# Kernel tuning notes

Hardware: AMD Instinct MI355X
Metric: run time of the kernel (lower is better)

## Reference

```python
import jax, jax.numpy as jnp
import numpy as np

D_MODEL = 1024
NUM_HEADS = 16
HEAD_DIM = D_MODEL // NUM_HEADS


def setup_inputs() -> dict:
    key = jax.random.key(0)
    ks = jax.random.split(key, 9)
    B, S, D = 4, 2048, D_MODEL
    scale = 1.0 / np.sqrt(D)
    x = jax.random.normal(ks[0], (B, S, D), dtype=jnp.float32)
    wq = jax.random.normal(ks[1], (D, D), dtype=jnp.float32) * scale
    wk = jax.random.normal(ks[2], (D, D), dtype=jnp.float32) * scale
    wv = jax.random.normal(ks[3], (D, D), dtype=jnp.float32) * scale
    wo = jax.random.normal(ks[4], (D, D), dtype=jnp.float32) * scale
    bq = jax.random.normal(ks[5], (D,), dtype=jnp.float32) * 0.02
    bk = jax.random.normal(ks[6], (D,), dtype=jnp.float32) * 0.02
    bv = jax.random.normal(ks[7], (D,), dtype=jnp.float32) * 0.02
    bo = jax.random.normal(ks[8], (D,), dtype=jnp.float32) * 0.02
    return {"x": x, "wq": wq, "bq": bq, "wk": wk, "bk": bk,
            "wv": wv, "bv": bv, "wo": wo, "bo": bo}


def _split_heads(t):  # [B,S,D] -> [B,H,S,Dh]
    B, S, _ = t.shape
    return t.reshape(B, S, NUM_HEADS, HEAD_DIM).transpose(0, 2, 1, 3)


def reference(x, wq, bq, wk, bk, wv, bv, wo, bo):
    B, S, D = x.shape
    q = _split_heads(x @ wq + bq)  # [B,H,S,Dh]
    k = _split_heads(x @ wk + bk)
    v = _split_heads(x @ wv + bv)
    scores = jnp.einsum("bhqd,bhkd->bhqk", q, k) / jnp.sqrt(
        jnp.asarray(HEAD_DIM, dtype=x.dtype))
    causal = jnp.tril(jnp.ones((S, S), dtype=bool))  # [S,S]
    scores = jnp.where(causal, scores, jnp.finfo(scores.dtype).min)
    attn = jax.nn.softmax(scores, axis=-1)
    ctx = jnp.einsum("bhqk,bhkd->bhqd", attn, v)  # [B,H,S,Dh]
    ctx = ctx.transpose(0, 2, 1, 3).reshape(B, S, D)
    return ctx @ wo + bo
```

## Files before the change

### kernel.cpp

```cpp
#include <hip/hip_runtime.h>
#include <hip/hip_bf16.h>
#include <stdint.h>

#define DMODEL 1024
#define NH 16
#define DH 64
#define BATCH 4
#define SEQ 2048

#if __has_builtin(__builtin_amdgcn_exp2f)
#define EXP2F(x) __builtin_amdgcn_exp2f(x)
#else
#define EXP2F(x) exp2f(x)
#endif

typedef __attribute__((ext_vector_type(8))) short short8;
typedef __attribute__((ext_vector_type(4))) float f32x4;
typedef __attribute__((ext_vector_type(4))) ushort ushort4v;

__device__ __forceinline__ ushort f2bf(float f) {
    union { float f; unsigned u; } v; v.f = f;
    unsigned r = v.u + 0x7fffu + ((v.u >> 16) & 1u);
    return (ushort)(r >> 16);
}

__global__ __launch_bounds__(256) void prep_inputs(
    const float* __restrict__ x, ushort* __restrict__ xbf,
    const float* __restrict__ s0, const float* __restrict__ s1,
    const float* __restrict__ s2, const float* __restrict__ s3,
    ushort* __restrict__ d0, ushort* __restrict__ d1,
    ushort* __restrict__ d2, ushort* __restrict__ d3) {
    __shared__ ushort tile[64][65];
    const int bid = blockIdx.x;
    if (bid < 4096) {
        const size_t i = ((size_t)bid * 256 + threadIdx.x) * 8;
        float4 a = *(const float4*)(x + i);
        float4 b = *(const float4*)(x + i + 4);
        short8 r;
        r[0] = (short)f2bf(a.x); r[1] = (short)f2bf(a.y);
        r[2] = (short)f2bf(a.z); r[3] = (short)f2bf(a.w);
        r[4] = (short)f2bf(b.x); r[5] = (short)f2bf(b.y);
        r[6] = (short)f2bf(b.z); r[7] = (short)f2bf(b.w);
        *(short8*)(xbf + i) = r;
        return;
    }
    const int r = bid - 4096;
    const int z = r >> 8;
    const float* src = (z == 0) ? s0 : (z == 1) ? s1 : (z == 2) ? s2 : s3;
    ushort* dst = (z == 0) ? d0 : (z == 1) ? d1 : (z == 2) ? d2 : d3;
    const int bx = (r & 15) * 64;
    const int by = ((r >> 4) & 15) * 64;
    const int tx = threadIdx.x & 63, ty = threadIdx.x >> 6;
    #pragma unroll
    for (int i = 0; i < 64; i += 4)
        tile[ty + i][tx] = f2bf(src[(size_t)(by + ty + i) * DMODEL + bx + tx]);
    __syncthreads();
    #pragma unroll
    for (int i = 0; i < 64; i += 4)
        dst[(size_t)(bx + ty + i) * DMODEL + by + tx] = tile[tx][ty + i];
}

#define BK 64
#define NT 16

template <int MODE>
__global__ __launch_bounds__(256, 2) void gemm_tile(
    const ushort* __restrict__ A, const ushort* __restrict__ Bt,
    const float* __restrict__ b0, const float* __restrict__ b1,
    const float* __restrict__ b2,
    void* __restrict__ o0v, void* __restrict__ o1v, void* __restrict__ o2v) {
    __shared__ __align__(16) ushort lds[32768];
    const int tid  = threadIdx.x;
    const int lane = tid & 63;
    const int wv   = tid >> 6;

    const int bid = blockIdx.x;
    const int by  = ((bid & 7) << 3) | ((bid >> 3) & 7);
    const int bx  = bid >> 6;
    const int mBase = by * 128, nBase = bx * 128;

    const int wm = (wv >> 1) * 64;
    const int wn = (wv & 1) * 64;
    const int frow = lane & 15;
    const int fq   = lane >> 4;
    const int r7x  = frow & 7;
    const int swk0 = (fq ^ r7x) << 3;
    const int swk1 = ((4 + fq) ^ r7x) << 3;

    const int trow = tid >> 3;
    const int tcho = ((tid & 7) ^ (trow & 7)) * 8;
    const ushort* gA = A  + (size_t)(mBase + trow) * DMODEL + tcho;
    const ushort* gB = Bt + (size_t)(nBase + trow) * DMODEL + tcho;
    const int ldsw = wv * 512;

    f32x4 acc[4][4];
    #pragma unroll
    for (int i = 0; i < 4; ++i)
        #pragma unroll
        for (int j = 0; j < 4; ++j) acc[i][j] = (f32x4){0.f, 0.f, 0.f, 0.f};

#define STG(gp, off) __builtin_amdgcn_global_load_lds( \
    (const __attribute__((address_space(1))) void*)(gp), \
    (__attribute__((address_space(3))) void*)&lds[(off) + ldsw], 16, 0, 0)
#define STAGE_A(sb, u, g) STG(gA + (size_t)(g) * 32 * DMODEL + (u) * BK, \
                              (sb) + (g) * 2048)
#define STAGE_B(sb, u, g) STG(gB + (size_t)(g) * 32 * DMODEL + (u) * BK, \
                              (sb) + 8192 + (g) * 2048)
#define STAGE_ALL(sb, u) { \
    STAGE_A(sb, u, 0); STAGE_A(sb, u, 1); STAGE_A(sb, u, 2); STAGE_A(sb, u, 3); \
    STAGE_B(sb, u, 0); STAGE_B(sb, u, 1); STAGE_B(sb, u, 2); STAGE_B(sb, u, 3); }

    STAGE_ALL(0, 0);
    asm volatile("s_waitcnt vmcnt(0)" ::: "memory");
    __builtin_amdgcn_s_barrier();

    #pragma unroll 1
    for (int u = 0; u < NT; ++u) {
        const int cb = (u & 1) * 16384;
        const int nb = 16384 - cb;

        if (u + 1 < NT) STAGE_ALL(nb, u + 1);

        const ushort* bufA = &lds[cb + wm * 64];
        const ushort* bufB = &lds[cb + 8192 + wn * 64];
        short8 af[4][2], bf[4][2];
        #pragma unroll
        for (int f = 0; f < 4; ++f) {
            const int ro = (f * 16 + frow) * 64;
            af[f][0] = *(const short8*)&bufA[ro + swk0];
            af[f][1] = *(const short8*)&bufA[ro + swk1];
        }
        #pragma unroll
        for (int j = 0; j < 4; ++j) {
            const int ro = (j * 16 + frow) * 64;
            bf[j][0] = *(const short8*)&bufB[ro + swk0];
            bf[j][1] = *(const short8*)&bufB[ro + swk1];
        }
        __builtin_amdgcn_s_setprio(1);
        #pragma unroll
        for (int f = 0; f < 4; ++f)
            #pragma unroll
            for (int j = 0; j < 4; ++j)
                #pragma unroll
                for (int ks = 0; ks < 2; ++ks)
                    acc[f][j] = __builtin_amdgcn_mfma_f32_16x16x32_bf16(
                        af[f][ks], bf[j][ks], acc[f][j], 0, 0, 0);
        __builtin_amdgcn_s_setprio(0);

        asm volatile("s_waitcnt vmcnt(0)" ::: "memory");
        __builtin_amdgcn_s_barrier();
    }
#undef STG
#undef STAGE_A
#undef STAGE_B
#undef STAGE_ALL

    const int orow = fq * 4;
    const int ocol = frow;

    if (MODE == 1) {
        #pragma unroll
        for (int i = 0; i < 4; ++i)
            #pragma unroll
            for (int j = 0; j < 4; ++j)
                #pragma unroll
                for (int r = 0; r < 4; ++r) {
                    const int m = mBase + wm + i * 16 + orow + r;
                    const int n = nBase + wn + j * 16 + ocol;
                    ((float*)o0v)[(size_t)m * DMODEL + n] = acc[i][j][r] + b0[n];
                }
        return;
    }

    __syncthreads();
    ushort* o0 = (ushort*)o0v; ushort* o1 = (ushort*)o1v; ushort* o2 = (ushort*)o2v;
    ushort* sw = &lds[wv * 1152];
    const int mat = nBase >> 10;
    const int nb0 = (nBase & 1023) + wn;
    const int hb  = nb0 >> 6;
    const float* bp = (mat == 0) ? b0 : ((mat == 1) ? b1 : b2);
    float bj[4];
    #pragma unroll
    for (int j = 0; j < 4; ++j) bj[j] = bp[nb0 + j * 16 + ocol];
    const int mrow = mBase + wm;
    const int bbq = mrow >> 11;
    const int s0w = mrow & 2047;
    const float qscale = (mat == 0) ? 0.1803368801f : 1.0f;

    if (mat < 2) {
        ushort* obase = ((mat == 0) ? o0 : o1) +
                        ((size_t)(bbq * NH + hb) * SEQ + s0w) * DH;
        const int row = lane >> 2, cc = lane & 3;
        #pragma unroll
        for (int i = 0; i < 4; ++i) {
            #pragma unroll
            for (int j = 0; j < 4; ++j)
                #pragma unroll
                for (int r = 0; r < 4; ++r)
                    sw[(orow + r) * 72 + j * 16 + ocol] =
                        f2bf((acc[i][j][r] + bj[j]) * qscale);
            asm volatile("s_waitcnt lgkmcnt(0)" ::: "memory");
            #pragma unroll
            for (int p = 0; p < 2; ++p) {
                short8 v8 = *(const short8*)&sw[row * 72 + cc * 8 + p * 32];
                *(short8*)&obase[(size_t)(i * 16 + row) * DH + cc * 8 + p * 32] = v8;
            }
            asm volatile("s_waitcnt lgkmcnt(0)" ::: "memory");
        }
    } else {
        const int rowd = lane >> 2, scl = lane & 3;
        #pragma unroll
        for (int j = 0; j < 4; ++j) {
            #pragma unroll
            for (int ii = 0; ii < 4; ++ii)
                #pragma unroll
                for (int r = 0; r < 4; ++r)
                    sw[ocol * 72 + ii * 16 + orow + r] = f2bf(acc[ii][j][r] + bj[j]);
            asm volatile("s_waitcnt lgkmcnt(0)" ::: "memory");
            ushort* vbase = o2 + ((size_t)(bbq * NH + hb) * DH + j * 16 + rowd) * SEQ + s0w;
            #pragma unroll
            for (int p = 0; p < 2; ++p) {
                short8 v8 = *(const short8*)&sw[rowd * 72 + scl * 8 + p * 32];
                *(short8*)&vbase[scl * 8 + p * 32] = v8;
            }
            asm volatile("s_waitcnt lgkmcnt(0)" ::: "memory");
        }
    }
}

#define PSTR 72
__global__ __launch_bounds__(512, 2) void flash_attn(
    const ushort* __restrict__ Q, const ushort* __restrict__ K,
    const ushort* __restrict__ Vt, ushort* __restrict__ ctx) {
    __shared__ __align__(16) ushort Ks[3][4096];
    __shared__ __align__(16) ushort Vs[3][4096];
    __shared__ __align__(16) ushort plds[8][16 * PSTR];
    const int tid  = threadIdx.x;
    const int lane = tid & 63;
    const int wv   = tid >> 6;
    const int bh   = blockIdx.x & 63;
    const int Jp   = blockIdx.x >> 6;
    const int bb = bh >> 4, h = bh & 15;

    const ushort* Qb = Q + (size_t)bh * SEQ * DH;
    const ushort* Kb = K + (size_t)bh * SEQ * DH;
    const ushort* Vb = Vt + (size_t)bh * DH * SEQ;

    const int frow = lane & 15;
    const int fq   = lane >> 4;
    const int trow = tid >> 3;
    const int tcho = ((tid & 7) ^ (trow & 7)) * 8;
    const int ldsw = wv * 512;

    short8 ones;
    #pragma unroll
    for (int i = 0; i < 8; ++i) ones[i] = (short)0x3F80;

#define FA_STG(gp, lp) __builtin_amdgcn_global_load_lds( \
    (const __attribute__((address_space(1))) void*)(gp), \
    (__attribute__((address_space(3))) void*)(lp), 16, 0, 0)
#define FA_STAGE(kt, buf) { \
    FA_STG(Kb + (size_t)((kt) * 64 + trow) * DH + tcho, &Ks[buf][ldsw]); \
    FA_STG(Vb + (size_t)trow * SEQ + (kt) * 64 + tcho, &Vs[buf][ldsw]); }

    #pragma unroll 1
    for (int half = 0; half < 2; ++half) {
        const int J = half ? (15 - Jp) : Jp;
        const int ktmax = 2 * J + 1;
        const int q0 = J * 128 + (wv >> 2) * 64 + (wv & 3) * 16;
        const int qmax = q0 + 15;

        short8 qf[2];
        #pragma unroll
        for (int ks = 0; ks < 2; ++ks)
            qf[ks] = *(const short8*)&Qb[(size_t)(q0 + frow) * DH + ks * 32 + fq * 8];

        f32x4 o[4], lacc;
        #pragma unroll
        for (int t = 0; t < 4; ++t) o[t] = (f32x4){0.f, 0.f, 0.f, 0.f};
        lacc = (f32x4){0.f, 0.f, 0.f, 0.f};

        FA_STAGE(0, 0);
        FA_STAGE(1, 1);
        asm volatile("s_waitcnt vmcnt(2)" ::: "memory");
        __builtin_amdgcn_s_barrier();

        #pragma unroll 1
        for (int kt = 0; kt <= ktmax; ++kt) {
            const int k0 = kt * 64;
            const int cur = kt % 3;
            const bool more = (kt + 2 <= ktmax);
            if (more) FA_STAGE(kt + 2, (kt + 2) % 3);
            const ushort* Ksc = Ks[cur];
            const ushort* Vsc = Vs[cur];

            if (k0 <= qmax) {
            if (k0 + 64 <= q0) {
                f32x4 sacc[4];
                #pragma unroll
                for (int nt = 0; nt < 4; ++nt) sacc[nt] = (f32x4){0.f, 0.f, 0.f, 0.f};
                #pragma unroll
                for (int nt = 0; nt < 4; ++nt) {
                    const int row = nt * 16 + frow, r7 = row & 7;
                    #pragma unroll
                    for (int ks = 0; ks < 2; ++ks) {
                        short8 kf = *(const short8*)
                            &Ksc[(row >> 3) * 512 + r7 * 64 + (((ks * 4 + fq) ^ r7) * 8)];
                        sacc[nt] = __builtin_amdgcn_mfma_f32_16x16x32_bf16(kf, qf[ks],
                                                                          sacc[nt], 0, 0, 0);
                    }
                }
                #pragma unroll
                for (int nt = 0; nt < 4; ++nt) {
                    float p0 = EXP2F(sacc[nt][0]);
                    float p1 = EXP2F(sacc[nt][1]);
                    float p2 = EXP2F(sacc[nt][2]);
                    float p3 = EXP2F(sacc[nt][3]);
                    uint2 dw;
                    dw.x = __builtin_amdgcn_perm(__float_as_uint(p1), __float_as_uint(p0),
                                                 0x07060302u);
                    dw.y = __builtin_amdgcn_perm(__float_as_uint(p3), __float_as_uint(p2),
                                                 0x07060302u);
                    *(uint2*)&plds[wv][frow * PSTR + nt * 16 + fq * 4] = dw;
                }
                asm volatile("s_waitcnt lgkmcnt(0)" ::: "memory");
                #pragma unroll
                for (int kc = 0; kc < 2; ++kc) {
                    short8 pf = *(const short8*)&plds[wv][frow * PSTR + kc * 32 + fq * 8];
                    lacc = __builtin_amdgcn_mfma_f32_16x16x32_bf16(ones, pf, lacc, 0, 0, 0);
                    __builtin_amdgcn_s_setprio(1);
                    #pragma unroll
                    for (int t = 0; t < 4; ++t) {
                        const int row = t * 16 + frow, r7 = row & 7;
                        short8 vf = *(const short8*)
                            &Vsc[(row >> 3) * 512 + r7 * 64 + (((kc * 4 + fq) ^ r7) * 8)];
                        o[t] = __builtin_amdgcn_mfma_f32_16x16x32_bf16(vf, pf, o[t], 0, 0, 0);
                    }
                    __builtin_amdgcn_s_setprio(0);
                }
            } else {
                const int qrow = q0 + frow;
                f32x4 sacc[4];
                #pragma unroll
                for (int nt = 0; nt < 4; ++nt) sacc[nt] = (f32x4){0.f, 0.f, 0.f, 0.f};
                #pragma unroll
                for (int nt = 0; nt < 4; ++nt)
                    if (k0 + nt * 16 <= qmax) {
                        const int row = nt * 16 + frow, r7 = row & 7;
                        #pragma unroll
                        for (int ks = 0; ks < 2; ++ks) {
                            short8 kf = *(const short8*)
                                &Ksc[(row >> 3) * 512 + r7 * 64 + (((ks * 4 + fq) ^ r7) * 8)];
                            sacc[nt] = __builtin_amdgcn_mfma_f32_16x16x32_bf16(kf, qf[ks],
                                                                              sacc[nt], 0, 0, 0);
                        }
                    }
                #pragma unroll
                for (int nt = 0; nt < 4; ++nt) {
                    uint2 dw; dw.x = 0u; dw.y = 0u;
                    if (k0 + nt * 16 <= qmax) {
                        float pp[4];
                        #pragma unroll
                        for (int r = 0; r < 4; ++r) {
                            const float e = EXP2F(sacc[nt][r]);
                            pp[r] = (k0 + nt * 16 + fq * 4 + r <= qrow) ? e : 0.f;
                        }
                        dw.x = __builtin_amdgcn_perm(__float_as_uint(pp[1]),
                                                     __float_as_uint(pp[0]), 0x07060302u);
                        dw.y = __builtin_amdgcn_perm(__float_as_uint(pp[3]),
                                                     __float_as_uint(pp[2]), 0x07060302u);
                    }
                    *(uint2*)&plds[wv][frow * PSTR + nt * 16 + fq * 4] = dw;
                }
                asm volatile("s_waitcnt lgkmcnt(0)" ::: "memory");
                #pragma unroll
                for (int kc = 0; kc < 2; ++kc) {
                    if (k0 + kc * 32 <= qmax) {
                        short8 pf = *(const short8*)&plds[wv][frow * PSTR + kc * 32 + fq * 8];
                        lacc = __builtin_amdgcn_mfma_f32_16x16x32_bf16(ones, pf, lacc, 0, 0, 0);
                        #pragma unroll
                        for (int t = 0; t < 4; ++t) {
                            const int row = t * 16 + frow, r7 = row & 7;
                            short8 vf = *(const short8*)
                                &Vsc[(row >> 3) * 512 + r7 * 64 + (((kc * 4 + fq) ^ r7) * 8)];
                            o[t] = __builtin_amdgcn_mfma_f32_16x16x32_bf16(vf, pf, o[t], 0, 0, 0);
                        }
                    }
                }
            }
            }

            if (more) { asm volatile("s_waitcnt lgkmcnt(0) vmcnt(2)" ::: "memory"); }
            else      { asm volatile("s_waitcnt lgkmcnt(0) vmcnt(0)" ::: "memory"); }
            __builtin_amdgcn_s_barrier();
        }

        const float inv = 1.0f / lacc[0];
        const int qrow = q0 + frow;
        ushort* cp = ctx + (size_t)(bb * SEQ + qrow) * DMODEL + h * DH;
        #pragma unroll
        for (int t = 0; t < 4; ++t) {
            ushort4v ov;
            #pragma unroll
            for (int r = 0; r < 4; ++r) ov[r] = f2bf(o[t][r] * inv);
            *(ushort4v*)&cp[t * 16 + fq * 4] = ov;
        }
    }
#undef FA_STG
#undef FA_STAGE
}

extern "C" void kernel_launch(void* const* d_in, const int* in_sizes, int n_in,
                              void* d_out, int out_size, void* d_ws, size_t ws_size,
                              hipStream_t stream) {
    const float* x  = (const float*)d_in[0];
    const float* wq = (const float*)d_in[1];
    const float* bq = (const float*)d_in[2];
    const float* wk = (const float*)d_in[3];
    const float* bk = (const float*)d_in[4];
    const float* wvp = (const float*)d_in[5];
    const float* bv = (const float*)d_in[6];
    const float* wo = (const float*)d_in[7];
    const float* bo = (const float*)d_in[8];
    float* out = (float*)d_out;
    ushort* ws = (ushort*)d_ws;

    const size_t QSZ = (size_t)BATCH * NH * SEQ * DH;
    ushort* xbf   = ws;
    ushort* qws   = ws + QSZ;
    ushort* kws   = ws + 2 * QSZ;
    ushort* vtws  = ws + 3 * QSZ;
    ushort* ctxws = ws + 4 * QSZ;
    ushort* wtqkv = ws + 5 * QSZ;
    ushort* wto   = wtqkv + 3 * (size_t)DMODEL * DMODEL;

    dim3 tb(256);
    prep_inputs<<<dim3(5120), tb, 0, stream>>>(
        x, xbf, wq, wk, wvp, wo,
        wtqkv, wtqkv + (size_t)DMODEL * DMODEL, wtqkv + 2 * (size_t)DMODEL * DMODEL, wto);

    gemm_tile<0><<<dim3(1536), tb, 0, stream>>>(xbf, wtqkv, bq, bk, bv,
                                                qws, kws, vtws);
    flash_attn<<<dim3(512), dim3(512), 0, stream>>>(qws, kws, vtws, ctxws);
    gemm_tile<1><<<dim3(512), tb, 0, stream>>>(ctxws, wto, bo, nullptr, nullptr,
                                               out, nullptr, nullptr);
}
```

Measured before the change: 220.0 us.

## Give each flash-attention wave two query tiles to reuse K/V fragments

The attention block shrinks from 8 to 4 waves. Each wave now handles 32 query rows as two 16-row tiles, so every K and V fragment read from LDS feeds two MFMAs instead of one. Each thread issues twice as many global-to-LDS staging loads per tile, and the vmcnt waits are adjusted to match. The aim is to halve LDS fragment traffic per MFMA. The cost is higher register pressure and fewer waves per block to hide latency.

```diff
diff --git a/kernel.cpp b/kernel.cpp
--- a/kernel.cpp
+++ b/kernel.cpp
@@ -229,12 +229,12 @@
 }
 
 #define PSTR 72
-__global__ __launch_bounds__(512, 2) void flash_attn(
+__global__ __launch_bounds__(256, 2) void flash_attn(
     const ushort* __restrict__ Q, const ushort* __restrict__ K,
     const ushort* __restrict__ Vt, ushort* __restrict__ ctx) {
     __shared__ __align__(16) ushort Ks[3][4096];
     __shared__ __align__(16) ushort Vs[3][4096];
-    __shared__ __align__(16) ushort plds[8][16 * PSTR];
+    __shared__ __align__(16) ushort plds[4][2][16 * PSTR];
     const int tid  = threadIdx.x;
     const int lane = tid & 63;
     const int wv   = tid >> 6;
@@ -261,28 +261,36 @@
     (__attribute__((address_space(3))) void*)(lp), 16, 0, 0)
 #define FA_STAGE(kt, buf) { \
     FA_STG(Kb + (size_t)((kt) * 64 + trow) * DH + tcho, &Ks[buf][ldsw]); \
-    FA_STG(Vb + (size_t)trow * SEQ + (kt) * 64 + tcho, &Vs[buf][ldsw]); }
+    FA_STG(Kb + (size_t)((kt) * 64 + 32 + trow) * DH + tcho, &Ks[buf][2048 + ldsw]); \
+    FA_STG(Vb + (size_t)trow * SEQ + (kt) * 64 + tcho, &Vs[buf][ldsw]); \
+    FA_STG(Vb + (size_t)(32 + trow) * SEQ + (kt) * 64 + tcho, &Vs[buf][2048 + ldsw]); }
 
     #pragma unroll 1
     for (int half = 0; half < 2; ++half) {
         const int J = half ? (15 - Jp) : Jp;
         const int ktmax = 2 * J + 1;
-        const int q0 = J * 128 + (wv >> 2) * 64 + (wv & 3) * 16;
-        const int qmax = q0 + 15;
-
-        short8 qf[2];
-        #pragma unroll
-        for (int ks = 0; ks < 2; ++ks)
-            qf[ks] = *(const short8*)&Qb[(size_t)(q0 + frow) * DH + ks * 32 + fq * 8];
-
-        f32x4 o[4], lacc;
-        #pragma unroll
-        for (int t = 0; t < 4; ++t) o[t] = (f32x4){0.f, 0.f, 0.f, 0.f};
-        lacc = (f32x4){0.f, 0.f, 0.f, 0.f};
+        const int q0 = J * 128 + wv * 32;
+        const int qmax0 = q0 + 15, qmax1 = q0 + 31;
+
+        short8 qf[2][2];
+        #pragma unroll
+        for (int qt = 0; qt < 2; ++qt)
+            #pragma unroll
+            for (int ks = 0; ks < 2; ++ks)
+                qf[qt][ks] = *(const short8*)
+                    &Qb[(size_t)(q0 + qt * 16 + frow) * DH + ks * 32 + fq * 8];
+
+        f32x4 o[2][4], lacc[2];
+        #pragma unroll
+        for (int qt = 0; qt < 2; ++qt) {
+            #pragma unroll
+            for (int t = 0; t < 4; ++t) o[qt][t] = (f32x4){0.f, 0.f, 0.f, 0.f};
+            lacc[qt] = (f32x4){0.f, 0.f, 0.f, 0.f};
+        }
 
         FA_STAGE(0, 0);
         FA_STAGE(1, 1);
-        asm volatile("s_waitcnt vmcnt(2)" ::: "memory");
+        asm volatile("s_waitcnt vmcnt(4)" ::: "memory");
         __builtin_amdgcn_s_barrier();
 
         #pragma unroll 1
@@ -294,11 +302,14 @@
             const ushort* Ksc = Ks[cur];
             const ushort* Vsc = Vs[cur];
 
-            if (k0 <= qmax) {
+            if (k0 <= qmax1) {
             if (k0 + 64 <= q0) {
-                f32x4 sacc[4];
-                #pragma unroll
-                for (int nt = 0; nt < 4; ++nt) sacc[nt] = (f32x4){0.f, 0.f, 0.f, 0.f};
+                f32x4 sacc[2][4];
+                #pragma unroll
+                for (int qt = 0; qt < 2; ++qt)
+                    #pragma unroll
+                    for (int nt = 0; nt < 4; ++nt)
+                        sacc[qt][nt] = (f32x4){0.f, 0.f, 0.f, 0.f};
                 #pragma unroll
                 for (int nt = 0; nt < 4; ++nt) {
                     const int row = nt * 16 + frow, r7 = row & 7;
@@ -306,104 +317,130 @@
                     for (int ks = 0; ks < 2; ++ks) {
                         short8 kf = *(const short8*)
                             &Ksc[(row >> 3) * 512 + r7 * 64 + (((ks * 4 + fq) ^ r7) * 8)];
-                        sacc[nt] = __builtin_amdgcn_mfma_f32_16x16x32_bf16(kf, qf[ks],
-                                                                          sacc[nt], 0, 0, 0);
+                        sacc[0][nt] = __builtin_amdgcn_mfma_f32_16x16x32_bf16(
+                            kf, qf[0][ks], sacc[0][nt], 0, 0, 0);
+                        sacc[1][nt] = __builtin_amdgcn_mfma_f32_16x16x32_bf16(
+                            kf, qf[1][ks], sacc[1][nt], 0, 0, 0);
                     }
                 }
                 #pragma unroll
-                for (int nt = 0; nt < 4; ++nt) {
-                    float p0 = EXP2F(sacc[nt][0]);
-                    float p1 = EXP2F(sacc[nt][1]);
-                    float p2 = EXP2F(sacc[nt][2]);
-                    float p3 = EXP2F(sacc[nt][3]);
-                    uint2 dw;
-                    dw.x = __builtin_amdgcn_perm(__float_as_uint(p1), __float_as_uint(p0),
-                                                 0x07060302u);
-                    dw.y = __builtin_amdgcn_perm(__float_as_uint(p3), __float_as_uint(p2),
-                                                 0x07060302u);
-                    *(uint2*)&plds[wv][frow * PSTR + nt * 16 + fq * 4] = dw;
-                }
+                for (int qt = 0; qt < 2; ++qt)
+                    #pragma unroll
+                    for (int nt = 0; nt < 4; ++nt) {
+                        float p0 = EXP2F(sacc[qt][nt][0]);
+                        float p1 = EXP2F(sacc[qt][nt][1]);
+                        float p2 = EXP2F(sacc[qt][nt][2]);
+                        float p3 = EXP2F(sacc[qt][nt][3]);
+                        uint2 dw;
+                        dw.x = __builtin_amdgcn_perm(__float_as_uint(p1),
+                                                     __float_as_uint(p0), 0x07060302u);
+                        dw.y = __builtin_amdgcn_perm(__float_as_uint(p3),
+                                                     __float_as_uint(p2), 0x07060302u);
+                        *(uint2*)&plds[wv][qt][frow * PSTR + nt * 16 + fq * 4] = dw;
+                    }
                 asm volatile("s_waitcnt lgkmcnt(0)" ::: "memory");
                 #pragma unroll
                 for (int kc = 0; kc < 2; ++kc) {
-                    short8 pf = *(const short8*)&plds[wv][frow * PSTR + kc * 32 + fq * 8];
-                    lacc = __builtin_amdgcn_mfma_f32_16x16x32_bf16(ones, pf, lacc, 0, 0, 0);
+                    short8 pf0 = *(const short8*)&plds[wv][0][frow * PSTR + kc * 32 + fq * 8];
+                    short8 pf1 = *(const short8*)&plds[wv][1][frow * PSTR + kc * 32 + fq * 8];
+                    lacc[0] = __builtin_amdgcn_mfma_f32_16x16x32_bf16(ones, pf0, lacc[0], 0, 0, 0);
+                    lacc[1] = __builtin_amdgcn_mfma_f32_16x16x32_bf16(ones, pf1, lacc[1], 0, 0, 0);
                     __builtin_amdgcn_s_setprio(1);
                     #pragma unroll
                     for (int t = 0; t < 4; ++t) {
                         const int row = t * 16 + frow, r7 = row & 7;
                         short8 vf = *(const short8*)
                             &Vsc[(row >> 3) * 512 + r7 * 64 + (((kc * 4 + fq) ^ r7) * 8)];
-                        o[t] = __builtin_amdgcn_mfma_f32_16x16x32_bf16(vf, pf, o[t], 0, 0, 0);
+                        o[0][t] = __builtin_amdgcn_mfma_f32_16x16x32_bf16(vf, pf0, o[0][t], 0, 0, 0);
+                        o[1][t] = __builtin_amdgcn_mfma_f32_16x16x32_bf16(vf, pf1, o[1][t], 0, 0, 0);
                     }
                     __builtin_amdgcn_s_setprio(0);
                 }
             } else {
-                const int qrow = q0 + frow;
-                f32x4 sacc[4];
-                #pragma unroll
-                for (int nt = 0; nt < 4; ++nt) sacc[nt] = (f32x4){0.f, 0.f, 0.f, 0.f};
+                f32x4 sacc[2][4];
+                #pragma unroll
+                for (int qt = 0; qt < 2; ++qt)
+                    #pragma unroll
+                    for (int nt = 0; nt < 4; ++nt)
+                        sacc[qt][nt] = (f32x4){0.f, 0.f, 0.f, 0.f};
                 #pragma unroll
                 for (int nt = 0; nt < 4; ++nt)
-                    if (k0 + nt * 16 <= qmax) {
+                    if (k0 + nt * 16 <= qmax1) {
                         const int row = nt * 16 + frow, r7 = row & 7;
                         #pragma unroll
                         for (int ks = 0; ks < 2; ++ks) {
                             short8 kf = *(const short8*)
                                 &Ksc[(row >> 3) * 512 + r7 * 64 + (((ks * 4 + fq) ^ r7) * 8)];
-                            sacc[nt] = __builtin_amdgcn_mfma_f32_16x16x32_bf16(kf, qf[ks],
-                                                                              sacc[nt], 0, 0, 0);
+                            sacc[1][nt] = __builtin_amdgcn_mfma_f32_16x16x32_bf16(
+                                kf, qf[1][ks], sacc[1][nt], 0, 0, 0);
+                            if (k0 + nt * 16 <= qmax0)
+                                sacc[0][nt] = __builtin_amdgcn_mfma_f32_16x16x32_bf16(
+                                    kf, qf[0][ks], sacc[0][nt], 0, 0, 0);
                         }
                     }
                 #pragma unroll
-                for (int nt = 0; nt < 4; ++nt) {
-                    uint2 dw; dw.x = 0u; dw.y = 0u;
-                    if (k0 + nt * 16 <= qmax) {
-                        float pp[4];
-                        #pragma unroll
-                        for (int r = 0; r < 4; ++r) {
-                            const float e = EXP2F(sacc[nt][r]);
-                            pp[r] = (k0 + nt * 16 + fq * 4 + r <= qrow) ? e : 0.f;
+                for (int qt = 0; qt < 2; ++qt) {
+                    const int qmaxq = q0 + qt * 16 + 15;
+                    const int qrowq = q0 + qt * 16 + frow;
+                    #pragma unroll
+                    for (int nt = 0; nt < 4; ++nt) {
+                        uint2 dw; dw.x = 0u; dw.y = 0u;
+                        if (k0 + nt * 16 <= qmaxq) {
+                            float pp[4];
+                            #pragma unroll
+                            for (int r = 0; r < 4; ++r) {
+                                const float e = EXP2F(sacc[qt][nt][r]);
+                                pp[r] = (k0 + nt * 16 + fq * 4 + r <= qrowq) ? e : 0.f;
+                            }
+                            dw.x = __builtin_amdgcn_perm(__float_as_uint(pp[1]),
+                                                         __float_as_uint(pp[0]), 0x07060302u);
+                            dw.y = __builtin_amdgcn_perm(__float_as_uint(pp[3]),
+                                                         __float_as_uint(pp[2]), 0x07060302u);
                         }
-                        dw.x = __builtin_amdgcn_perm(__float_as_uint(pp[1]),
-                                                     __float_as_uint(pp[0]), 0x07060302u);
-                        dw.y = __builtin_amdgcn_perm(__float_as_uint(pp[3]),
-                                                     __float_as_uint(pp[2]), 0x07060302u);
-                    }
-                    *(uint2*)&plds[wv][frow * PSTR + nt * 16 + fq * 4] = dw;
+                        *(uint2*)&plds[wv][qt][frow * PSTR + nt * 16 + fq * 4] = dw;
+                    }
                 }
                 asm volatile("s_waitcnt lgkmcnt(0)" ::: "memory");
                 #pragma unroll
                 for (int kc = 0; kc < 2; ++kc) {
-                    if (k0 + kc * 32 <= qmax) {
-                        short8 pf = *(const short8*)&plds[wv][frow * PSTR + kc * 32 + fq * 8];
-                        lacc = __builtin_amdgcn_mfma_f32_16x16x32_bf16(ones, pf, lacc, 0, 0, 0);
-                        #pragma unroll
-                        for (int t = 0; t < 4; ++t) {
-                            const int row = t * 16 + frow, r7 = row & 7;
+                    short8 pf0 = *(const short8*)&plds[wv][0][frow * PSTR + kc * 32 + fq * 8];
+                    short8 pf1 = *(const short8*)&plds[wv][1][frow * PSTR + kc * 32 + fq * 8];
+                    const bool u0 = (k0 + kc * 32 <= qmax0);
+                    const bool u1 = (k0 + kc * 32 <= qmax1);
+                    if (u0) lacc[0] = __builtin_amdgcn_mfma_f32_16x16x32_bf16(ones, pf0, lacc[0], 0, 0, 0);
+                    if (u1) lacc[1] = __builtin_amdgcn_mfma_f32_16x16x32_bf16(ones, pf1, lacc[1], 0, 0, 0);
+                    #pragma unroll
+                    for (int t = 0; t < 4; ++t) {
+                        const int row = t * 16 + frow, r7 = row & 7;
+                        if (u1) {
                             short8 vf = *(const short8*)
                                 &Vsc[(row >> 3) * 512 + r7 * 64 + (((kc * 4 + fq) ^ r7) * 8)];
-                            o[t] = __builtin_amdgcn_mfma_f32_16x16x32_bf16(vf, pf, o[t], 0, 0, 0);
+                            o[1][t] = __builtin_amdgcn_mfma_f32_16x16x32_bf16(vf, pf1, o[1][t], 0, 0, 0);
+                            if (u0)
+                                o[0][t] = __builtin_amdgcn_mfma_f32_16x16x32_bf16(vf, pf0, o[0][t], 0, 0, 0);
                         }
                     }
                 }
             }
             }
 
-            if (more) { asm volatile("s_waitcnt lgkmcnt(0) vmcnt(2)" ::: "memory"); }
+            if (more) { asm volatile("s_waitcnt lgkmcnt(0) vmcnt(4)" ::: "memory"); }
             else      { asm volatile("s_waitcnt lgkmcnt(0) vmcnt(0)" ::: "memory"); }
             __builtin_amdgcn_s_barrier();
         }
 
-        const float inv = 1.0f / lacc[0];
-        const int qrow = q0 + frow;
-        ushort* cp = ctx + (size_t)(bb * SEQ + qrow) * DMODEL + h * DH;
-        #pragma unroll
-        for (int t = 0; t < 4; ++t) {
-            ushort4v ov;
-            #pragma unroll
-            for (int r = 0; r < 4; ++r) ov[r] = f2bf(o[t][r] * inv);
-            *(ushort4v*)&cp[t * 16 + fq * 4] = ov;
+        #pragma unroll
+        for (int qt = 0; qt < 2; ++qt) {
+            const float inv = 1.0f / lacc[qt][0];
+            const int qrow = q0 + qt * 16 + frow;
+            ushort* cp = ctx + (size_t)(bb * SEQ + qrow) * DMODEL + h * DH;
+            #pragma unroll
+            for (int t = 0; t < 4; ++t) {
+                ushort4v ov;
+                #pragma unroll
+                for (int r = 0; r < 4; ++r) ov[r] = f2bf(o[qt][t][r] * inv);
+                *(ushort4v*)&cp[t * 16 + fq * 4] = ov;
+            }
         }
     }
 #undef FA_STG
@@ -441,7 +478,7 @@
 
     gemm_tile<0><<<dim3(1536), tb, 0, stream>>>(xbf, wtqkv, bq, bk, bv,
                                                 qws, kws, vtws);
-    flash_attn<<<dim3(512), dim3(512), 0, stream>>>(qws, kws, vtws, ctxws);
+    flash_attn<<<dim3(512), tb, 0, stream>>>(qws, kws, vtws, ctxws);
     gemm_tile<1><<<dim3(512), tb, 0, stream>>>(ctxws, wto, bo, nullptr, nullptr,
                                                out, nullptr, nullptr);
 }
```

After: 234.4 us. +6.5%, slower.
